# Kernel tuning notes

Hardware: AMD Instinct MI355X
Metric: run time of the kernel (lower is better)

Reference implementation:

```python
import jax, jax.numpy as jnp
import numpy as np

LAYERS, BLOCKS = 10, 3
N_BLK = LAYERS * BLOCKS
RC, SC, K = 128, 128, 2
IN_CH, COND_CH, OUT_CH = 256, 80, 256
DILATIONS = tuple(2 ** (i % LAYERS) for i in range(N_BLK))
INV_SQRT2 = 0.70710678118


def conv1x1(x, w, b):
    # x: [B, I, T], w: [O, I], b: [O] -> [B, O, T]
    return jnp.einsum('oi,bit->bot', w, x) + b[None, :, None]


def causal_conv(x, w, b, dilation):
    # x: [B, C, T], w: [O, I, K]; left-pad by (K-1)*d == torch pad-both + right slice
    pad = (w.shape[2] - 1) * dilation
    y = jax.lax.conv_general_dilated(
        x, w, window_strides=(1,), padding=[(pad, 0)],
        rhs_dilation=(dilation,), dimension_numbers=('NCH', 'OIH', 'NCH'))
    return y + b[None, :, None]


def setup_inputs() -> dict:
    key = jax.random.key(0)
    ks = jax.random.split(key, 20)
    s = 0.05
    B, T = 2, 8000
    inp = {
        'x': jax.random.normal(ks[0], (B, IN_CH, T), jnp.float32),
        'condition': jax.random.normal(ks[1], (B, COND_CH, T), jnp.float32),
        'input_w': jax.random.normal(ks[2], (RC, IN_CH), jnp.float32) * s,
        'input_b': jax.random.normal(ks[3], (RC,), jnp.float32) * s,
        'dil_w': jax.random.normal(ks[4], (N_BLK, RC, RC, K), jnp.float32) * s,
        'dil_b': jax.random.normal(ks[5], (N_BLK, RC), jnp.float32) * s,
        'gate_w': jax.random.normal(ks[6], (N_BLK, RC, RC), jnp.float32) * s,
        'gate_b': jax.random.normal(ks[7], (N_BLK, RC), jnp.float32) * s,
        'cond_w': jax.random.normal(ks[8], (N_BLK, RC, COND_CH), jnp.float32) * s,
        'cond_b': jax.random.normal(ks[9], (N_BLK, RC), jnp.float32) * s,
        'condg_w': jax.random.normal(ks[10], (N_BLK, RC, COND_CH), jnp.float32) * s,
        'condg_b': jax.random.normal(ks[11], (N_BLK, RC), jnp.float32) * s,
        'res_w': jax.random.normal(ks[12], (N_BLK, RC, RC), jnp.float32) * s,
        'res_b': jax.random.normal(ks[13], (N_BLK, RC), jnp.float32) * s,
        'skip_w': jax.random.normal(ks[14], (N_BLK, SC, RC), jnp.float32) * s,
        'skip_b': jax.random.normal(ks[15], (N_BLK, SC), jnp.float32) * s,
        'out1_w': jax.random.normal(ks[16], (SC, SC), jnp.float32) * s,
        'out1_b': jax.random.normal(ks[17], (SC,), jnp.float32) * s,
        'out2_w': jax.random.normal(ks[18], (OUT_CH, SC), jnp.float32) * s,
        'out2_b': jax.random.normal(ks[19], (OUT_CH,), jnp.float32) * s,
    }
    return inp


def reference(x, condition, input_w, input_b, dil_w, dil_b, gate_w, gate_b,
              cond_w, cond_b, condg_w, condg_b, res_w, res_b,
              skip_w, skip_b, out1_w, out1_b, out2_w, out2_b):
    h = conv1x1(x, input_w, input_b)  # [B, RC, T]
    skip = jnp.zeros_like(conv1x1(h, skip_w[0], skip_b[0]) * 0)  # [B, SC, T]
    for i, d in enumerate(DILATIONS):
        a = causal_conv(h, dil_w[i], dil_b[i], d) + conv1x1(condition, cond_w[i], cond_b[i])
        g = conv1x1(h, gate_w[i], gate_b[i]) + conv1x1(condition, condg_w[i], condg_b[i])
        out = jnp.tanh(a) * jax.nn.sigmoid(g)
        h = (h + conv1x1(out, res_w[i], res_b[i])) * INV_SQRT2
        skip = skip + conv1x1(out, skip_w[i], skip_b[i])
    y = jax.nn.relu(conv1x1(skip, out1_w, out1_b))
    return conv1x1(y, out2_w, out2_b)  # [B, 256, T]
```

## Files before the change

### kernel.cpp

```cpp
#include <hip/hip_runtime.h>

#define T_LEN 8000
#define NTPB 125
#define NBLK 250
#define NLAYER 30
#define GUARD 512
#define HROWS (GUARD + T_LEN)
#define SLAB (HROWS * 128)
#define INV_SQRT2 0.70710678118f

typedef short bf16x8 __attribute__((ext_vector_type(8)));
typedef unsigned uint2v __attribute__((ext_vector_type(2)));
typedef unsigned uint4v __attribute__((ext_vector_type(4)));
typedef float f32x4 __attribute__((ext_vector_type(4)));

#define R_HT  0
#define R_OUT 8192
#define R_CND 16384
#define WB0   22528
#define WB1   38912
#define LDS_SHORTS 55296

#define KLINE 4096
#define LS 106496
#define C1 16384
#define C2 32768
#define C3 49152
#define C4 57344
#define C5 73728
#define C6 90112
#define IN_OFF   3194880
#define OUT1_OFF 3227648
#define OUT2_OFF 3244032

__device__ __forceinline__ unsigned short f2bf_u(float f) {
    union { float f; unsigned u; } v; v.f = f;
    unsigned u = v.u + 0x7FFFu + ((v.u >> 16) & 1u);
    return (unsigned short)(u >> 16);
}
__device__ __forceinline__ short f2bf(float f) { return (short)f2bf_u(f); }

__device__ __forceinline__ unsigned cvtpk(float lo, float hi) {
    unsigned r;
    asm("v_cvt_pk_bf16_f32 %0, %1, %2" : "=v"(r) : "v"(lo), "v"(hi));
    return r;
}

__device__ __forceinline__ float gated_act(float av, float gv) {
    float e  = __expf(-2.f * fabsf(av));
    float th = (1.f - e) * __builtin_amdgcn_rcpf(1.f + e);
    th = (av < 0.f) ? -th : th;
    float sg = __builtin_amdgcn_rcpf(1.f + __expf(-gv));
    return th * sg;
}

__device__ __forceinline__ void ldg16_sc1(bf16x8* d, const short* p) {
    asm volatile("global_load_dwordx4 %0, %1, off sc1" : "=v"(*d) : "v"(p));
}
__device__ __forceinline__ void stg8_sc1(short* p, uint2v v) {
    asm volatile("global_store_dwordx2 %0, %1, off sc1" : : "v"(p), "v"(v) : "memory");
}
__device__ __forceinline__ void st_flag(int* p, int v) {
    __hip_atomic_store(p, v, __ATOMIC_RELAXED, __HIP_MEMORY_SCOPE_AGENT);
}
__device__ __forceinline__ void wait_ge(const int* p, int v) {
    while (__hip_atomic_load(p, __ATOMIC_RELAXED, __HIP_MEMORY_SCOPE_AGENT) < v)
        __builtin_amdgcn_s_sleep(1);
}

__device__ __forceinline__ f32x4 mfma_(bf16x8 a, bf16x8 b, f32x4 c) {
    return __builtin_amdgcn_mfma_f32_16x16x32_bf16(a, b, c, 0, 0, 0);
}

__device__ __forceinline__ void gload_lds16(const short* g, short* l) {
    __builtin_amdgcn_global_load_lds(
        (const __attribute__((address_space(1))) unsigned int*)g,
        (__attribute__((address_space(3))) unsigned int*)l, 16, 0, 0);
}
__device__ __forceinline__ void stageW2(const short* src, short* dst, int wv, int lane) {
    gload_lds16(src + wv * 512 + lane * 8, dst + wv * 512);
    gload_lds16(src + (16 + wv) * 512 + lane * 8, dst + (16 + wv) * 512);
}
__device__ __forceinline__ void stageW1(const short* src, short* dst, int wv, int lane) {
    gload_lds16(src + wv * 512 + lane * 8, dst + wv * 512);
}

template<int NP>
__device__ __forceinline__ void pairN(const short* wb, const short* sm, int boff,
                                      int ks0, int lg, int awoff,
                                      f32x4* ac0, f32x4* ac1)
{
#pragma unroll
    for (int p = 0; p < NP; ++p) {
        bf16x8 B = *(const bf16x8*)&sm[boff + ((ks0 + p) * 4 + lg) * 512];
#pragma unroll
        for (int mt = 0; mt < 2; ++mt) {
            bf16x8 a0 = *(const bf16x8*)&wb[p * 8192 + awoff + mt * 512];
            ac0[mt] = mfma_(a0, B, ac0[mt]);
            bf16x8 a1 = *(const bf16x8*)&wb[p * 8192 + 4096 + awoff + mt * 512];
            ac1[mt] = mfma_(a1, B, ac1[mt]);
        }
    }
}
template<int NP>
__device__ __forceinline__ void singleN(const short* wb, const short* sm, int boff,
                                        int ks0, int lg, int awoff, f32x4* ac)
{
#pragma unroll
    for (int p = 0; p < NP; ++p) {
        bf16x8 B = *(const bf16x8*)&sm[boff + ((ks0 + p) * 4 + lg) * 512];
#pragma unroll
        for (int mt = 0; mt < 2; ++mt) {
            bf16x8 a = *(const bf16x8*)&wb[p * 4096 + awoff + mt * 512];
            ac[mt] = mfma_(a, B, ac[mt]);
        }
    }
}

__global__ __launch_bounds__(256) void k_pack(
    const float* __restrict__ dil_w, const float* __restrict__ gate_w,
    const float* __restrict__ cond_w, const float* __restrict__ condg_w,
    const float* __restrict__ res_w, const float* __restrict__ skip_w,
    const float* __restrict__ input_w, const float* __restrict__ out1_w,
    const float* __restrict__ out2_w,
    const float* __restrict__ dil_b, const float* __restrict__ cond_b,
    const float* __restrict__ gate_b, const float* __restrict__ condg_b,
    short* __restrict__ wp, short* __restrict__ hbt, int* __restrict__ flg)
{
    int gid = blockIdx.x * 256 + threadIdx.x;
    if (gid < 512) flg[gid] = 0;
    {
        int g2 = gid - 512;
        if (g2 >= 0 && g2 < 262144) {
            unsigned* hb32 = (unsigned*)hbt;
            int slab = g2 >> 15, off = g2 & 32767;
            hb32[(size_t)slab * (SLAB / 2) + off] = 0u;
        }
    }
    if (gid >= 6400 * 64) return;
    int fid = gid >> 6, lane = gid & 63;
    int lr = lane & 15, lg = lane >> 4;
    float v[8];
    if (fid < 6240) {
        int layer = fid / 208;
        int r = fid - layer * 208;
        int kl = r >> 3, f = r & 7;
        int m = f * 16 + lr;
        size_t mi = (size_t)layer * 128 + m;
        int mat, ks;
        if      (kl < 8)  { mat = (kl & 1) ? 2 : 1; ks = kl >> 1; }
        else if (kl < 14) { mat = (kl & 1) ? 4 : 3; ks = (kl - 8) >> 1; }
        else if (kl < 18) { mat = 0; ks = kl - 14; }
        else              { mat = (kl & 1) ? 6 : 5; ks = (kl - 18) >> 1; }
        int kb = ks * 32 + lg * 8;
#pragma unroll
        for (int e = 0; e < 8; ++e) {
            int k = kb + e;
            float val;
            switch (mat) {
                case 0:  val = dil_w[(mi * 128 + k) * 2];     break;
                case 1:  val = dil_w[(mi * 128 + k) * 2 + 1]; break;
                case 2:  val = gate_w[mi * 128 + k]; break;
                case 3:  val = (k < 80) ? cond_w[mi * 80 + k]
                               : ((k == 80) ? dil_b[mi] + cond_b[mi] : 0.f); break;
                case 4:  val = (k < 80) ? condg_w[mi * 80 + k]
                               : ((k == 80) ? gate_b[mi] + condg_b[mi] : 0.f); break;
                case 5:  val = res_w[mi * 128 + k]; break;
                default: val = skip_w[mi * 128 + k]; break;
            }
            v[e] = val;
        }
    } else if (fid < 6304) {
        int f = fid - 6240; int ks = f >> 3, fr = f & 7;
        int m = fr * 16 + lr; int kb = ks * 32 + lg * 8;
#pragma unroll
        for (int e = 0; e < 8; ++e) v[e] = input_w[(size_t)m * 256 + kb + e];
    } else if (fid < 6336) {
        int f = fid - 6304; int ks = f >> 3, fr = f & 7;
        int m = fr * 16 + lr; int kb = ks * 32 + lg * 8;
#pragma unroll
        for (int e = 0; e < 8; ++e) v[e] = out1_w[(size_t)m * 128 + kb + e];
    } else {
        int f = fid - 6336; int mt = f & 15; int ks = f >> 4;
        int m = mt * 16 + lr; int kb = ks * 32 + lg * 8;
#pragma unroll
        for (int e = 0; e < 8; ++e) v[e] = out2_w[(size_t)m * 128 + kb + e];
    }
    short* dst = wp + (size_t)fid * 512 + lane * 8;
#pragma unroll
    for (int e = 0; e < 8; ++e) dst[e] = f2bf(v[e]);
}

__global__ __launch_bounds__(1024, 4) void k_wavenet(
    const float* __restrict__ x, const float* __restrict__ cond,
    const short* __restrict__ wp, short* __restrict__ hbt,
    const float* __restrict__ ib, const float* __restrict__ rbias,
    const float* __restrict__ sbias, const float* __restrict__ b1,
    const float* __restrict__ b2, float* __restrict__ outp,
    int* __restrict__ rdy, int* __restrict__ dn)
{
    __shared__ __align__(16) short sm[LDS_SHORTS];

    const int tid  = threadIdx.x;
    const int lane = tid & 63;
    const int wv   = __builtin_amdgcn_readfirstlane(tid >> 6);
    const int wm   = wv & 3;
    const int wn   = wv >> 2;
    const int lr   = lane & 15, lg = lane >> 4;
    const int bidx = blockIdx.x;
    const int b    = bidx / NTPB;
    const int ti   = bidx - b * NTPB;
    const int t0   = ti * 64;
    const int tl   = wn * 16 + lr;
    const int tg   = t0 + tl;
    const int tl8  = tl * 8;
    const int lane8 = lane * 8;
    const int awoff = wm * 1024 + lane8;
    const int chA  = wm * 32 + lg * 4;
    const int kbA  = wm * 4 + (lg >> 1);
    const int e0   = (lg & 1) * 4;

    stageW2(wp + IN_OFF, (short*)&sm[WB0], wv, lane);
    stageW2(wp + IN_OFF + 16384, (short*)&sm[WB1], wv, lane);
    {
        const float* xb = x + (size_t)b * 256 * T_LEN + t0 + lane;
#pragma unroll
        for (int it = 0; it < 2; ++it) {
            int kb = wv * 2 + it;
            unsigned pk[4];
#pragma unroll
            for (int e = 0; e < 4; ++e)
                pk[e] = cvtpk(xb[(size_t)(kb * 8 + 2 * e) * T_LEN],
                              xb[(size_t)(kb * 8 + 2 * e + 1) * T_LEN]);
            *(uint4v*)&sm[(kb * 64 + lane) * 8] = *(uint4v*)pk;
        }
        if (wv < 12) {
            const float* cb = cond + (size_t)b * 80 * T_LEN + t0 + lane;
            unsigned pk[4];
#pragma unroll
            for (int e = 0; e < 4; ++e) {
                int c0 = wv * 8 + 2 * e, c1 = c0 + 1;
                float v0 = (c0 < 80) ? cb[(size_t)c0 * T_LEN] : ((c0 == 80) ? 1.f : 0.f);
                float v1 = (c1 < 80) ? cb[(size_t)c1 * T_LEN] : 0.f;
                pk[e] = cvtpk(v0, v1);
            }
            *(uint4v*)&sm[R_CND + (wv * 64 + lane) * 8] = *(uint4v*)pk;
        }
    }
    __syncthreads();

    f32x4 hres[2] = {{0.f,0.f,0.f,0.f},{0.f,0.f,0.f,0.f}};
    {
        f32x4 acc[2] = {{0.f,0.f,0.f,0.f},{0.f,0.f,0.f,0.f}};
        singleN<4>((const short*)&sm[WB0], sm, tl8, 0, lg, awoff, acc);
        singleN<4>((const short*)&sm[WB1], sm, tl8, 4, lg, awoff, acc);
#pragma unroll
        for (int mt = 0; mt < 2; ++mt) {
            int cb0 = chA + mt * 16;
            f32x4 bv = {ib[cb0], ib[cb0 + 1], ib[cb0 + 2], ib[cb0 + 3]};
            hres[mt] = acc[mt] + bv;
        }
    }
    __syncthreads();
    {
        short* hrow = hbt + (size_t)b * SLAB + (size_t)(GUARD + tg) * 128 + chA;
#pragma unroll
        for (int mt = 0; mt < 2; ++mt) {
            uint2v hv = {cvtpk(hres[mt][0], hres[mt][1]), cvtpk(hres[mt][2], hres[mt][3])};
            stg8_sc1(hrow + mt * 16, hv);
            *(uint2v*)&sm[R_HT + ((kbA + mt * 2) * 64 + tl) * 8 + e0] = hv;
        }
    }
    __syncthreads();
    if (tid == 0) st_flag(&rdy[bidx], 1);

    f32x4 skp[2] = {{0.f,0.f,0.f,0.f},{0.f,0.f,0.f,0.f}};

    for (int li = 0; li < NLAYER; ++li) {
        const int d   = 1 << (li % 10);
        const int ksh = (d + 63) >> 6;
        const short* wl  = wp + (size_t)li * LS;
        const short* hcb = hbt + (size_t)((li & 3) * 2 + b) * SLAB;
        short*       hnb = hbt + (size_t)(((li + 1) & 3) * 2 + b) * SLAB;

        stageW2(wl, (short*)&sm[WB0], wv, lane);
        __syncthreads();
        if (lane == 0 && ti >= ksh) wait_ge(&rdy[bidx - ksh], li + 1);
        bf16x8 Bg[4];
        {
            const short* hr = hcb + (size_t)(GUARD + tg - d) * 128 + lg * 8;
#pragma unroll
            for (int ks = 0; ks < 4; ++ks) ldg16_sc1(&Bg[ks], hr + ks * 32);
        }
        stageW2(wl + C1, (short*)&sm[WB1], wv, lane);
        f32x4 aa[2] = {{0.f,0.f,0.f,0.f},{0.f,0.f,0.f,0.f}};
        f32x4 ag[2] = {{0.f,0.f,0.f,0.f},{0.f,0.f,0.f,0.f}};
        pairN<2>((const short*)&sm[WB0], sm, R_HT + tl8, 0, lg, awoff, aa, ag);
        __syncthreads();
        if (tid == 0) st_flag(&dn[bidx], li + 1);
        stageW2(wl + C2, (short*)&sm[WB0], wv, lane);
        pairN<2>((const short*)&sm[WB1], sm, R_HT + tl8, 2, lg, awoff, aa, ag);
        __syncthreads();
        stageW1(wl + C3, (short*)&sm[WB1], wv, lane);
        pairN<2>((const short*)&sm[WB0], sm, R_CND + tl8, 0, lg, awoff, aa, ag);
        __syncthreads();
        stageW2(wl + C4, (short*)&sm[WB0], wv, lane);
        pairN<1>((const short*)&sm[WB1], sm, R_CND + tl8, 2, lg, awoff, aa, ag);
        __syncthreads();
        stageW2(wl + C5, (short*)&sm[WB1], wv, lane);
        {
            const short* wb = (const short*)&sm[WB0];
#pragma unroll
            for (int ks = 0; ks < 4; ++ks) {
#pragma unroll
                for (int mt = 0; mt < 2; ++mt) {
                    bf16x8 a = *(const bf16x8*)&wb[ks * 4096 + awoff + mt * 512];
                    aa[mt] = mfma_(a, Bg[ks], aa[mt]);
                }
            }
        }
#pragma unroll
        for (int mt = 0; mt < 2; ++mt) {
            uint2v ov = {cvtpk(gated_act(aa[mt][0], ag[mt][0]), gated_act(aa[mt][1], ag[mt][1])),
                         cvtpk(gated_act(aa[mt][2], ag[mt][2]), gated_act(aa[mt][3], ag[mt][3]))};
            *(uint2v*)&sm[R_OUT + ((kbA + mt * 2) * 64 + tl) * 8 + e0] = ov;
        }
        __syncthreads();
        stageW2(wl + C6, (short*)&sm[WB0], wv, lane);
        f32x4 ar[2]  = {{0.f,0.f,0.f,0.f},{0.f,0.f,0.f,0.f}};
        f32x4 as2[2] = {{0.f,0.f,0.f,0.f},{0.f,0.f,0.f,0.f}};
        pairN<2>((const short*)&sm[WB1], sm, R_OUT + tl8, 0, lg, awoff, ar, as2);
        __syncthreads();
        pairN<2>((const short*)&sm[WB0], sm, R_OUT + tl8, 2, lg, awoff, ar, as2);

        const float* rbl = rbias + li * 128 + chA;
        const float* sbl = sbias + li * 128 + chA;
#pragma unroll
        for (int mt = 0; mt < 2; ++mt) {
            f32x4 rbv = {rbl[mt*16], rbl[mt*16+1], rbl[mt*16+2], rbl[mt*16+3]};
            f32x4 sbv = {sbl[mt*16], sbl[mt*16+1], sbl[mt*16+2], sbl[mt*16+3]};
            skp[mt]  = skp[mt] + as2[mt] + sbv;
            hres[mt] = (hres[mt] + ar[mt] + rbv) * INV_SQRT2;
        }
        if (li < NLAYER - 1) {
            if (lane == 0 && li >= 3) {
                int d3 = 1 << ((li - 3) % 10);
                int k3 = (d3 + 63) >> 6;
                if (ti + k3 < NTPB) wait_ge(&dn[bidx + k3], li - 2);
            }
            short* hrow = hnb + (size_t)(GUARD + tg) * 128 + chA;
#pragma unroll
            for (int mt = 0; mt < 2; ++mt) {
                uint2v hv = {cvtpk(hres[mt][0], hres[mt][1]), cvtpk(hres[mt][2], hres[mt][3])};
                stg8_sc1(hrow + mt * 16, hv);
                *(uint2v*)&sm[R_HT + ((kbA + mt * 2) * 64 + tl) * 8 + e0] = hv;
            }
        }
        __syncthreads();
        if (tid == 0 && li < NLAYER - 1) st_flag(&rdy[bidx], li + 2);
    }

#pragma unroll
    for (int mt = 0; mt < 2; ++mt) {
        uint2v sv = {cvtpk(skp[mt][0], skp[mt][1]), cvtpk(skp[mt][2], skp[mt][3])};
        *(uint2v*)&sm[R_HT + ((kbA + mt * 2) * 64 + tl) * 8 + e0] = sv;
    }
    stageW2(wp + OUT1_OFF, (short*)&sm[WB0], wv, lane);
    stageW2(wp + OUT2_OFF, (short*)&sm[WB1], wv, lane);
    __syncthreads();
    f32x4 ay[2] = {{0.f,0.f,0.f,0.f},{0.f,0.f,0.f,0.f}};
    singleN<4>((const short*)&sm[WB0], sm, R_HT + tl8, 0, lg, awoff, ay);
#pragma unroll
    for (int mt = 0; mt < 2; ++mt) {
        int cb0 = chA + mt * 16;
        float y0 = fmaxf(ay[mt][0] + b1[cb0],     0.f);
        float y1 = fmaxf(ay[mt][1] + b1[cb0 + 1], 0.f);
        float y2 = fmaxf(ay[mt][2] + b1[cb0 + 2], 0.f);
        float y3 = fmaxf(ay[mt][3] + b1[cb0 + 3], 0.f);
        uint2v yv = {cvtpk(y0, y1), cvtpk(y2, y3)};
        *(uint2v*)&sm[R_OUT + ((kbA + mt * 2) * 64 + tl) * 8 + e0] = yv;
    }
    __syncthreads();
    stageW2(wp + OUT2_OFF + 16384, (short*)&sm[WB0], wv, lane);
    f32x4 ao[4] = {{0.f,0.f,0.f,0.f},{0.f,0.f,0.f,0.f},
                   {0.f,0.f,0.f,0.f},{0.f,0.f,0.f,0.f}};
    {
        const short* wb = (const short*)&sm[WB1];
#pragma unroll
        for (int ksp = 0; ksp < 2; ++ksp) {
            bf16x8 B = *(const bf16x8*)&sm[R_OUT + tl8 + (ksp * 4 + lg) * 512];
#pragma unroll
            for (int mt = 0; mt < 4; ++mt) {
                int fg = 4 * wm + mt;
                bf16x8 A = *(const bf16x8*)&wb[(ksp * 2 + (fg >> 3)) * 4096 + (fg & 7) * 512 + lane8];
                ao[mt] = mfma_(A, B, ao[mt]);
            }
        }
    }
    __syncthreads();
    {
        const short* wb = (const short*)&sm[WB0];
#pragma unroll
        for (int ksp = 0; ksp < 2; ++ksp) {
            bf16x8 B = *(const bf16x8*)&sm[R_OUT + tl8 + ((2 + ksp) * 4 + lg) * 512];
#pragma unroll
            for (int mt = 0; mt < 4; ++mt) {
                int fg = 4 * wm + mt;
                bf16x8 A = *(const bf16x8*)&wb[(ksp * 2 + (fg >> 3)) * 4096 + (fg & 7) * 512 + lane8];
                ao[mt] = mfma_(A, B, ao[mt]);
            }
        }
    }
#pragma unroll
    for (int mt = 0; mt < 4; ++mt) {
        int ch2 = wm * 64 + mt * 16 + lg * 4;
        float* op = outp + ((size_t)(b * 256 + ch2)) * T_LEN + tg;
        op[0]         = ao[mt][0] + b2[ch2];
        op[T_LEN]     = ao[mt][1] + b2[ch2 + 1];
        op[2 * T_LEN] = ao[mt][2] + b2[ch2 + 2];
        op[3 * T_LEN] = ao[mt][3] + b2[ch2 + 3];
    }
}

extern "C" void kernel_launch(void* const* d_in, const int* in_sizes, int n_in,
                              void* d_out, int out_size, void* d_ws, size_t ws_size,
                              hipStream_t stream)
{
    const float* x       = (const float*)d_in[0];
    const float* cond    = (const float*)d_in[1];
    const float* input_w = (const float*)d_in[2];
    const float* input_b = (const float*)d_in[3];
    const float* dil_w   = (const float*)d_in[4];
    const float* dil_b   = (const float*)d_in[5];
    const float* gate_w  = (const float*)d_in[6];
    const float* gate_b  = (const float*)d_in[7];
    const float* cond_w  = (const float*)d_in[8];
    const float* cond_b  = (const float*)d_in[9];
    const float* condg_w = (const float*)d_in[10];
    const float* condg_b = (const float*)d_in[11];
    const float* res_w   = (const float*)d_in[12];
    const float* res_b   = (const float*)d_in[13];
    const float* skip_w  = (const float*)d_in[14];
    const float* skip_b  = (const float*)d_in[15];
    const float* out1_w  = (const float*)d_in[16];
    const float* out1_b  = (const float*)d_in[17];
    const float* out2_w  = (const float*)d_in[18];
    const float* out2_b  = (const float*)d_in[19];
    float* outp = (float*)d_out;

    short* wpk = (short*)d_ws;
    short* hbt = wpk + (size_t)6400 * 512;
    int*   flg = (int*)(hbt + (size_t)8 * SLAB);
    int*   rdy = flg;
    int*   dn  = flg + 256;

    k_pack<<<1600, 256, 0, stream>>>(dil_w, gate_w, cond_w, condg_w, res_w, skip_w,
                                     input_w, out1_w, out2_w,
                                     dil_b, cond_b, gate_b, condg_b, wpk, hbt, flg);

    void* args[] = {(void*)&x, (void*)&cond, (void*)&wpk, (void*)&hbt,
                    (void*)&input_b, (void*)&res_b, (void*)&skip_b,
                    (void*)&out1_b, (void*)&out2_b, (void*)&outp,
                    (void*)&rdy, (void*)&dn};
    hipLaunchCooperativeKernel((void*)k_wavenet, dim3(NBLK), dim3(1024), args, 0, stream);
}
```

Before: 289.5 us.

## Restage layer weights into larger LDS buffers with fewer barriers and cross-layer prefetch

LDS weight staging moves from two 16K-short buffers refilled in 7 chunks per layer to two larger buffers (32K and 24K shorts) filled in 4 chunks. This roughly halves the __syncthreads per layer. The next layer's first weight chunk (dil+gate on h) is prefetched at the end of the current layer, using manual vmcnt/lgkmcnt waits and a raw s_barrier, so its global latency overlaps the inter-block flag handshake. In exchange LDS use grows from ~110KB to ~160KB, and the hand-written waitcnt accounting is fragile.

```diff
diff --git a/kernel.cpp b/kernel.cpp
--- a/kernel.cpp
+++ b/kernel.cpp
@@ -17,21 +17,21 @@
 #define R_HT  0
 #define R_OUT 8192
 #define R_CND 16384
-#define WB0   22528
-#define WB1   38912
-#define LDS_SHORTS 55296
-
-#define KLINE 4096
+#define WA    22528
+#define WB    55296
+#define LDS_SHORTS 79872
+
 #define LS 106496
-#define C1 16384
-#define C2 32768
-#define C3 49152
-#define C4 57344
-#define C5 73728
-#define C6 90112
+#define CH2 32768
+#define CH3 57344
+#define CH4 81920
 #define IN_OFF   3194880
 #define OUT1_OFF 3227648
 #define OUT2_OFF 3244032
+
+#define WAITV(N) asm volatile("s_waitcnt vmcnt(" #N ")" ::: "memory")
+#define LGKM0    asm volatile("s_waitcnt lgkmcnt(0)" ::: "memory")
+#define BAR      asm volatile("s_barrier" ::: "memory")
 
 __device__ __forceinline__ unsigned short f2bf_u(float f) {
     union { float f; unsigned u; } v; v.f = f;
@@ -45,7 +45,6 @@
     asm("v_cvt_pk_bf16_f32 %0, %1, %2" : "=v"(r) : "v"(lo), "v"(hi));
     return r;
 }
-
 __device__ __forceinline__ float gated_act(float av, float gv) {
     float e  = __expf(-2.f * fabsf(av));
     float th = (1.f - e) * __builtin_amdgcn_rcpf(1.f + e);
@@ -53,7 +52,6 @@
     float sg = __builtin_amdgcn_rcpf(1.f + __expf(-gv));
     return th * sg;
 }
-
 __device__ __forceinline__ void ldg16_sc1(bf16x8* d, const short* p) {
     asm volatile("global_load_dwordx4 %0, %1, off sc1" : "=v"(*d) : "v"(p));
 }
@@ -67,22 +65,21 @@
     while (__hip_atomic_load(p, __ATOMIC_RELAXED, __HIP_MEMORY_SCOPE_AGENT) < v)
         __builtin_amdgcn_s_sleep(1);
 }
-
 __device__ __forceinline__ f32x4 mfma_(bf16x8 a, bf16x8 b, f32x4 c) {
     return __builtin_amdgcn_mfma_f32_16x16x32_bf16(a, b, c, 0, 0, 0);
 }
-
 __device__ __forceinline__ void gload_lds16(const short* g, short* l) {
     __builtin_amdgcn_global_load_lds(
         (const __attribute__((address_space(1))) unsigned int*)g,
         (__attribute__((address_space(3))) unsigned int*)l, 16, 0, 0);
 }
-__device__ __forceinline__ void stageW2(const short* src, short* dst, int wv, int lane) {
-    gload_lds16(src + wv * 512 + lane * 8, dst + wv * 512);
-    gload_lds16(src + (16 + wv) * 512 + lane * 8, dst + (16 + wv) * 512);
-}
-__device__ __forceinline__ void stageW1(const short* src, short* dst, int wv, int lane) {
-    gload_lds16(src + wv * 512 + lane * 8, dst + wv * 512);
+template<int R>
+__device__ __forceinline__ void stageK(const short* src, short* dst, int wv, int lane) {
+#pragma unroll
+    for (int r = 0; r < R; ++r) {
+        int off = (r * 16 + wv) * 512;
+        gload_lds16(src + off + lane * 8, dst + off);
+    }
 }
 
 template<int NP>
@@ -220,8 +217,10 @@
     const int kbA  = wm * 4 + (lg >> 1);
     const int e0   = (lg & 1) * 4;
 
-    stageW2(wp + IN_OFF, (short*)&sm[WB0], wv, lane);
-    stageW2(wp + IN_OFF + 16384, (short*)&sm[WB1], wv, lane);
+    short* const wA = (short*)&sm[WA];
+    short* const wB = (short*)&sm[WB];
+
+    stageK<4>(wp + IN_OFF, wA, wv, lane);
     {
         const float* xb = x + (size_t)b * 256 * T_LEN + t0 + lane;
 #pragma unroll
@@ -252,8 +251,8 @@
     f32x4 hres[2] = {{0.f,0.f,0.f,0.f},{0.f,0.f,0.f,0.f}};
     {
         f32x4 acc[2] = {{0.f,0.f,0.f,0.f},{0.f,0.f,0.f,0.f}};
-        singleN<4>((const short*)&sm[WB0], sm, tl8, 0, lg, awoff, acc);
-        singleN<4>((const short*)&sm[WB1], sm, tl8, 4, lg, awoff, acc);
+        singleN<4>(wA, sm, tl8, 0, lg, awoff, acc);
+        singleN<4>(wA + 16384, sm, tl8, 4, lg, awoff, acc);
 #pragma unroll
         for (int mt = 0; mt < 2; ++mt) {
             int cb0 = chA + mt * 16;
@@ -271,6 +270,8 @@
             *(uint2v*)&sm[R_HT + ((kbA + mt * 2) * 64 + tl) * 8 + e0] = hv;
         }
     }
+    stageK<4>(wp, wA, wv, lane);
+    asm volatile("s_waitcnt vmcnt(0)" ::: "memory");
     __syncthreads();
     if (tid == 0) st_flag(&rdy[bidx], 1);
 
@@ -283,8 +284,7 @@
         const short* hcb = hbt + (size_t)((li & 3) * 2 + b) * SLAB;
         short*       hnb = hbt + (size_t)(((li + 1) & 3) * 2 + b) * SLAB;
 
-        stageW2(wl, (short*)&sm[WB0], wv, lane);
-        __syncthreads();
+        stageK<3>(wl + CH2, wB, wv, lane);
         if (lane == 0 && ti >= ksh) wait_ge(&rdy[bidx - ksh], li + 1);
         bf16x8 Bg[4];
         {
@@ -292,29 +292,23 @@
 #pragma unroll
             for (int ks = 0; ks < 4; ++ks) ldg16_sc1(&Bg[ks], hr + ks * 32);
         }
-        stageW2(wl + C1, (short*)&sm[WB1], wv, lane);
         f32x4 aa[2] = {{0.f,0.f,0.f,0.f},{0.f,0.f,0.f,0.f}};
         f32x4 ag[2] = {{0.f,0.f,0.f,0.f},{0.f,0.f,0.f,0.f}};
-        pairN<2>((const short*)&sm[WB0], sm, R_HT + tl8, 0, lg, awoff, aa, ag);
+        pairN<4>(wA, sm, R_HT + tl8, 0, lg, awoff, aa, ag);
         __syncthreads();
         if (tid == 0) st_flag(&dn[bidx], li + 1);
-        stageW2(wl + C2, (short*)&sm[WB0], wv, lane);
-        pairN<2>((const short*)&sm[WB1], sm, R_HT + tl8, 2, lg, awoff, aa, ag);
+
+        stageK<3>(wl + CH3, wA, wv, lane);
+        pairN<3>(wB, sm, R_CND + tl8, 0, lg, awoff, aa, ag);
         __syncthreads();
-        stageW1(wl + C3, (short*)&sm[WB1], wv, lane);
-        pairN<2>((const short*)&sm[WB0], sm, R_CND + tl8, 0, lg, awoff, aa, ag);
-        __syncthreads();
-        stageW2(wl + C4, (short*)&sm[WB0], wv, lane);
-        pairN<1>((const short*)&sm[WB1], sm, R_CND + tl8, 2, lg, awoff, aa, ag);
-        __syncthreads();
-        stageW2(wl + C5, (short*)&sm[WB1], wv, lane);
+
+        stageK<3>(wl + CH4, wB, wv, lane);
         {
-            const short* wb = (const short*)&sm[WB0];
 #pragma unroll
             for (int ks = 0; ks < 4; ++ks) {
 #pragma unroll
                 for (int mt = 0; mt < 2; ++mt) {
-                    bf16x8 a = *(const bf16x8*)&wb[ks * 4096 + awoff + mt * 512];
+                    bf16x8 a = *(const bf16x8*)&wA[ks * 4096 + awoff + mt * 512];
                     aa[mt] = mfma_(a, Bg[ks], aa[mt]);
                 }
             }
@@ -326,22 +320,24 @@
             *(uint2v*)&sm[R_OUT + ((kbA + mt * 2) * 64 + tl) * 8 + e0] = ov;
         }
         __syncthreads();
-        stageW2(wl + C6, (short*)&sm[WB0], wv, lane);
+
         f32x4 ar[2]  = {{0.f,0.f,0.f,0.f},{0.f,0.f,0.f,0.f}};
         f32x4 as2[2] = {{0.f,0.f,0.f,0.f},{0.f,0.f,0.f,0.f}};
-        pairN<2>((const short*)&sm[WB1], sm, R_OUT + tl8, 0, lg, awoff, ar, as2);
+        pairN<1>(wA + 16384, sm, R_OUT + tl8, 0, lg, awoff, ar, as2);
+        pairN<3>(wB, sm, R_OUT + tl8, 1, lg, awoff, ar, as2);
+        {
+            const float* rbl = rbias + li * 128 + chA;
+            const float* sbl = sbias + li * 128 + chA;
+#pragma unroll
+            for (int mt = 0; mt < 2; ++mt) {
+                f32x4 rbv = {rbl[mt*16], rbl[mt*16+1], rbl[mt*16+2], rbl[mt*16+3]};
+                f32x4 sbv = {sbl[mt*16], sbl[mt*16+1], sbl[mt*16+2], sbl[mt*16+3]};
+                skp[mt]  = skp[mt] + as2[mt] + sbv;
+                hres[mt] = (hres[mt] + ar[mt] + rbv) * INV_SQRT2;
+            }
+        }
         __syncthreads();
-        pairN<2>((const short*)&sm[WB0], sm, R_OUT + tl8, 2, lg, awoff, ar, as2);
-
-        const float* rbl = rbias + li * 128 + chA;
-        const float* sbl = sbias + li * 128 + chA;
-#pragma unroll
-        for (int mt = 0; mt < 2; ++mt) {
-            f32x4 rbv = {rbl[mt*16], rbl[mt*16+1], rbl[mt*16+2], rbl[mt*16+3]};
-            f32x4 sbv = {sbl[mt*16], sbl[mt*16+1], sbl[mt*16+2], sbl[mt*16+3]};
-            skp[mt]  = skp[mt] + as2[mt] + sbv;
-            hres[mt] = (hres[mt] + ar[mt] + rbv) * INV_SQRT2;
-        }
+
         if (li < NLAYER - 1) {
             if (lane == 0 && li >= 3) {
                 int d3 = 1 << ((li - 3) % 10);
@@ -355,9 +351,13 @@
                 stg8_sc1(hrow + mt * 16, hv);
                 *(uint2v*)&sm[R_HT + ((kbA + mt * 2) * 64 + tl) * 8 + e0] = hv;
             }
-        }
-        __syncthreads();
-        if (tid == 0 && li < NLAYER - 1) st_flag(&rdy[bidx], li + 2);
+            stageK<4>(wl + LS, wA, wv, lane);
+            WAITV(4);
+            LGKM0; BAR;
+            if (tid == 0) st_flag(&rdy[bidx], li + 2);
+        } else {
+            __syncthreads();
+        }
     }
 
 #pragma unroll
@@ -365,11 +365,12 @@
         uint2v sv = {cvtpk(skp[mt][0], skp[mt][1]), cvtpk(skp[mt][2], skp[mt][3])};
         *(uint2v*)&sm[R_HT + ((kbA + mt * 2) * 64 + tl) * 8 + e0] = sv;
     }
-    stageW2(wp + OUT1_OFF, (short*)&sm[WB0], wv, lane);
-    stageW2(wp + OUT2_OFF, (short*)&sm[WB1], wv, lane);
+    stageK<2>(wp + OUT1_OFF, wA, wv, lane);
+    stageK<2>(wp + OUT2_OFF, wA + 16384, wv, lane);
+    stageK<2>(wp + OUT2_OFF + 16384, wB, wv, lane);
     __syncthreads();
     f32x4 ay[2] = {{0.f,0.f,0.f,0.f},{0.f,0.f,0.f,0.f}};
-    singleN<4>((const short*)&sm[WB0], sm, R_HT + tl8, 0, lg, awoff, ay);
+    singleN<4>(wA, sm, R_HT + tl8, 0, lg, awoff, ay);
 #pragma unroll
     for (int mt = 0; mt < 2; ++mt) {
         int cb0 = chA + mt * 16;
@@ -381,32 +382,28 @@
         *(uint2v*)&sm[R_OUT + ((kbA + mt * 2) * 64 + tl) * 8 + e0] = yv;
     }
     __syncthreads();
-    stageW2(wp + OUT2_OFF + 16384, (short*)&sm[WB0], wv, lane);
     f32x4 ao[4] = {{0.f,0.f,0.f,0.f},{0.f,0.f,0.f,0.f},
                    {0.f,0.f,0.f,0.f},{0.f,0.f,0.f,0.f}};
     {
-        const short* wb = (const short*)&sm[WB1];
+        const short* w2a = wA + 16384;
+        const short* w2b = wB;
 #pragma unroll
         for (int ksp = 0; ksp < 2; ++ksp) {
             bf16x8 B = *(const bf16x8*)&sm[R_OUT + tl8 + (ksp * 4 + lg) * 512];
 #pragma unroll
             for (int mt = 0; mt < 4; ++mt) {
                 int fg = 4 * wm + mt;
-                bf16x8 A = *(const bf16x8*)&wb[(ksp * 2 + (fg >> 3)) * 4096 + (fg & 7) * 512 + lane8];
+                bf16x8 A = *(const bf16x8*)&w2a[(ksp * 2 + (fg >> 3)) * 4096 + (fg & 7) * 512 + lane8];
                 ao[mt] = mfma_(A, B, ao[mt]);
             }
         }
-    }
-    __syncthreads();
-    {
-        const short* wb = (const short*)&sm[WB0];
 #pragma unroll
         for (int ksp = 0; ksp < 2; ++ksp) {
             bf16x8 B = *(const bf16x8*)&sm[R_OUT + tl8 + ((2 + ksp) * 4 + lg) * 512];
 #pragma unroll
             for (int mt = 0; mt < 4; ++mt) {
                 int fg = 4 * wm + mt;
-                bf16x8 A = *(const bf16x8*)&wb[(ksp * 2 + (fg >> 3)) * 4096 + (fg & 7) * 512 + lane8];
+                bf16x8 A = *(const bf16x8*)&w2b[(ksp * 2 + (fg >> 3)) * 4096 + (fg & 7) * 512 + lane8];
                 ao[mt] = mfma_(A, B, ao[mt]);
             }
         }
@@ -462,5 +459,5 @@
                     (void*)&input_b, (void*)&res_b, (void*)&skip_b,
                     (void*)&out1_b, (void*)&out2_b, (void*)&outp,
                     (void*)&rdy, (void*)&dn};
-    hipLaunchCooperativeKernel((void*)k_wavenet, dim3(NBLK), dim3(1024), args, 0, stream);
-}
+    (void)hipLaunchCooperativeKernel((void*)k_wavenet, dim3(NBLK), dim3(1024), args, 0, stream);
+}
```

Measured after the change: 322.6 us. 1.11x slower.
